# Kernel optimization log

Measured on AMD Instinct MI355X. Metric: run time of the kernel, lower is better.

## Reference

```python
import jax, jax.numpy as jnp
import numpy as np

D_MODEL = 1024
N_HEADS = 16
D_FF = 512  # FeedForward default d_ff=512 (not overridden in EncoderLayer)
EPS = 1e-6


def _norm(x, alpha, bias):
    # Custom NormLayer: mean + UNBIASED variance (torch.var default, N-1 denom)
    mean = jnp.mean(x, axis=-1, keepdims=True)
    n = x.shape[-1]
    var = jnp.sum((x - mean) ** 2, axis=-1, keepdims=True) / (n - 1)
    return alpha * (x - mean) / jnp.sqrt(var + EPS) + bias


def setup_inputs() -> dict:
    key = jax.random.key(0)
    ks = jax.random.split(key, 12)
    s = 1.0 / np.sqrt(D_MODEL)
    inp = {
        "x": jax.random.normal(ks[0], (2, 2048, D_MODEL), dtype=jnp.float32),
        "Wq": jax.random.uniform(ks[1], (D_MODEL, D_MODEL), jnp.float32, -s, s),
        "bq": jnp.zeros((D_MODEL,), jnp.float32),
        "Wk": jax.random.uniform(ks[2], (D_MODEL, D_MODEL), jnp.float32, -s, s),
        "bk": jnp.zeros((D_MODEL,), jnp.float32),
        "Wv": jax.random.uniform(ks[3], (D_MODEL, D_MODEL), jnp.float32, -s, s),
        "bv": jnp.zeros((D_MODEL,), jnp.float32),
        "Wo": jax.random.uniform(ks[4], (D_MODEL, D_MODEL), jnp.float32, -s, s),
        "bo": jnp.zeros((D_MODEL,), jnp.float32),
        "alpha1": jnp.ones((D_MODEL,), jnp.float32),
        "beta1": jnp.zeros((D_MODEL,), jnp.float32),
        "alpha2": jnp.ones((D_MODEL,), jnp.float32),
        "beta2": jnp.zeros((D_MODEL,), jnp.float32),
        "W1": jax.random.uniform(ks[5], (D_MODEL, D_FF), jnp.float32, -s, s),
        "b1": jnp.zeros((D_FF,), jnp.float32),
        "W2": jax.random.uniform(ks[6], (D_FF, D_MODEL), jnp.float32, -1.0 / np.sqrt(D_FF), 1.0 / np.sqrt(D_FF)),
        "b2": jnp.zeros((D_MODEL,), jnp.float32),
    }
    return inp


def reference(x, Wq, bq, Wk, bk, Wv, bv, Wo, bo, alpha1, beta1, alpha2, beta2, W1, b1, W2, b2):
    B, S, D = x.shape
    H = N_HEADS
    dh = D // H
    # norm_1 applied to x, result feeds BOTH attention and the residual
    x = _norm(x, alpha1, beta1)
    # multihead attention (dropout = identity in eval)
    q = (x @ Wq + bq).reshape(B, S, H, dh)
    k = (x @ Wk + bk).reshape(B, S, H, dh)
    v = (x @ Wv + bv).reshape(B, S, H, dh)
    scores = jnp.einsum("bqhd,bkhd->bhqk", q, k) / jnp.sqrt(jnp.asarray(dh, x.dtype))
    attn = jax.nn.softmax(scores, axis=-1)
    o = jnp.einsum("bhqk,bkhd->bqhd", attn, v).reshape(B, S, D)
    o = o @ Wo + bo
    x = x + o
    # FFN on norm_2(x)
    h = _norm(x, alpha2, beta2)
    h = jax.nn.relu(h @ W1 + b1) @ W2 + b2
    return x + h
```

## Files before the change

kernel.cpp:

```cpp
#include <hip/hip_runtime.h>

typedef __bf16 bf16;
typedef __bf16 bf16x4 __attribute__((ext_vector_type(4)));
typedef __bf16 bf16x8 __attribute__((ext_vector_type(8)));
typedef float f32x4 __attribute__((ext_vector_type(4)));

#define D_MODEL 1024
#define SEQ 2048
#define NB 2
#define LOG2E 1.4426950408889634f

__device__ __forceinline__ void glds16(const bf16* g, bf16* l) {
    __builtin_amdgcn_global_load_lds(
        (const __attribute__((address_space(1))) void*)g,
        (__attribute__((address_space(3))) void*)l, 16, 0, 0);
}

__device__ __forceinline__ void tile_tcvt(
    const float* __restrict__ src, int rows, int cols, bf16* __restrict__ dst,
    int bx, int by, bf16 (*t)[72])
{
    int tid = threadIdx.x;
    int k0 = by * 64, n0 = bx * 64;
    int r = tid >> 2, c = (tid & 3) * 16;
    const float4* s = (const float4*)(src + (size_t)(k0 + r) * cols + n0 + c);
#pragma unroll
    for (int q = 0; q < 4; ++q) {
        float4 v = s[q];
        t[c + q * 4 + 0][r] = (bf16)v.x;
        t[c + q * 4 + 1][r] = (bf16)v.y;
        t[c + q * 4 + 2][r] = (bf16)v.z;
        t[c + q * 4 + 3][r] = (bf16)v.w;
    }
    __syncthreads();
    bf16* d = dst + (size_t)(n0 + r) * rows + k0 + c;
    *(bf16x8*)(d)     = *(const bf16x8*)&t[r][c];
    *(bf16x8*)(d + 8) = *(const bf16x8*)&t[r][c + 8];
}

__global__ __launch_bounds__(256) void prep_kernel(
    const float* __restrict__ Wq, const float* __restrict__ Wk,
    const float* __restrict__ Wv, const float* __restrict__ Wo,
    const float* __restrict__ W1, const float* __restrict__ W2,
    const float* __restrict__ bq, const float* __restrict__ bk,
    const float* __restrict__ bv,
    bf16* __restrict__ Wqkv_t, bf16* __restrict__ Wo_t,
    bf16* __restrict__ W1_t, bf16* __restrict__ W2_t,
    float* __restrict__ b_qkv)
{
    __shared__ bf16 t[64][72];
    int id = blockIdx.x;
    if (id < 1024) {
        int which = id >> 8, tile = id & 255;
        const float* src = which == 0 ? Wq : which == 1 ? Wk : which == 2 ? Wv : Wo;
        bf16* dst = which == 3 ? Wo_t : Wqkv_t + (size_t)which * 1024 * 1024;
        tile_tcvt(src, 1024, 1024, dst, tile & 15, tile >> 4, t);
    } else if (id < 1152) {
        int tile = id - 1024;
        tile_tcvt(W1, 1024, 512, W1_t, tile & 7, tile >> 3, t);
    } else if (id < 1280) {
        int tile = id - 1152;
        tile_tcvt(W2, 512, 1024, W2_t, tile & 15, tile >> 4, t);
    } else {
        int i = (id - 1280) * 256 + threadIdx.x;
        float v;
        if (i < 1024) v = bq[i];
        else if (i < 2048) v = bk[i - 1024];
        else v = bv[i - 2048];
        b_qkv[i] = v;
    }
}

__global__ __launch_bounds__(256) void norm_kernel(
    const float* __restrict__ X, const float* __restrict__ alpha,
    const float* __restrict__ beta, bf16* __restrict__ Y)
{
    int row = blockIdx.x;
    int tid = threadIdx.x;
    float4 v = ((const float4*)(X + (size_t)row * D_MODEL))[tid];
    float s = v.x + v.y + v.z + v.w;
    float ss = v.x*v.x + v.y*v.y + v.z*v.z + v.w*v.w;
#pragma unroll
    for (int off = 1; off < 64; off <<= 1) {
        s  += __shfl_xor(s, off, 64);
        ss += __shfl_xor(ss, off, 64);
    }
    __shared__ float sd[8];
    int wave = tid >> 6, lane = tid & 63;
    if (lane == 0) { sd[wave] = s; sd[4 + wave] = ss; }
    __syncthreads();
    s  = sd[0] + sd[1] + sd[2] + sd[3];
    ss = sd[4] + sd[5] + sd[6] + sd[7];
    float mean = s * (1.0f / 1024.0f);
    float var  = (ss - s * mean) * (1.0f / 1023.0f);
    float rs = rsqrtf(var + 1e-6f);
    float4 a = ((const float4*)alpha)[tid];
    float4 bt = ((const float4*)beta)[tid];
    bf16x4 o;
    o[0] = (bf16)(a.x * (v.x - mean) * rs + bt.x);
    o[1] = (bf16)(a.y * (v.y - mean) * rs + bt.y);
    o[2] = (bf16)(a.z * (v.z - mean) * rs + bt.z);
    o[3] = (bf16)(a.w * (v.w - mean) * rs + bt.w);
    *(bf16x4*)(Y + (size_t)row * D_MODEL + tid * 4) = o;
}

__global__ __launch_bounds__(256) void crelu_kernel(
    const float* __restrict__ p0, const float* __restrict__ p1,
    const float* __restrict__ b1, bf16* __restrict__ h1)
{
    int i = blockIdx.x * 256 + threadIdx.x;
    float4 a = ((const float4*)p0)[i];
    float4 b = ((const float4*)p1)[i];
    int col = (i * 4) & 511;
    float4 bb = *(const float4*)(b1 + col);
    bf16x4 o;
    o[0] = (bf16)fmaxf(a.x + b.x + bb.x, 0.0f);
    o[1] = (bf16)fmaxf(a.y + b.y + bb.y, 0.0f);
    o[2] = (bf16)fmaxf(a.z + b.z + bb.z, 0.0f);
    o[3] = (bf16)fmaxf(a.w + b.w + bb.w, 0.0f);
    ((bf16x4*)h1)[i] = o;
}

template <typename OutT, int BN, int KU, bool VFUSE, bool SPLITK>
__global__ __launch_bounds__(256) void gemm128(
    const bf16* __restrict__ A, const bf16* __restrict__ Bt,
    const float* __restrict__ bias, const bf16* __restrict__ Rb,
    const float* __restrict__ Rf, OutT* __restrict__ C, bf16* __restrict__ vT,
    int M, int N, int K, int lda, int relu)
{
    constexpr int NT = BN / 32;
    constexpr int ASTR = 128 * 32;
    constexpr int BSTR = BN * 32;
    __shared__ bf16 As[ASTR * KU];
    __shared__ bf16 Bs[BSTR * KU];

    int tid = threadIdx.x;
    int wave = tid >> 6, lane = tid & 63;
    int quad = lane >> 4, l16 = lane & 15;
    int m0 = blockIdx.y * 128, n0 = blockIdx.x * BN;
    int wm = (wave >> 1) * 64, wn = (wave & 1) * (BN / 2);
    int Keff = SPLITK ? (K >> 1) : K;
    int klo  = SPLITK ? blockIdx.z * Keff : 0;

    f32x4 acc[4][NT] = {};

    const bf16* ga = A  + (size_t)(m0 + (tid >> 2)) * lda + (tid & 3) * 8 + klo;
    const bf16* gb = Bt + (size_t)(n0 + (tid >> 2)) * K   + (tid & 3) * 8 + klo;
    bf16* lAs = As + wave * 512;
    bf16* lBs = Bs + wave * 512;

    for (int k0 = 0; k0 < Keff; k0 += 32 * KU) {
        __syncthreads();
#pragma unroll
        for (int u = 0; u < KU; ++u) {
            glds16(ga + k0 + u * 32, lAs + u * ASTR);
            glds16(ga + (size_t)64 * lda + k0 + u * 32, lAs + u * ASTR + 2048);
            glds16(gb + k0 + u * 32, lBs + u * BSTR);
            if (BN == 128) glds16(gb + (size_t)64 * K + k0 + u * 32, lBs + u * BSTR + 2048);
        }
        __syncthreads();
#pragma unroll
        for (int u = 0; u < KU; ++u) {
            bf16x8 af[4], bfr[NT];
#pragma unroll
            for (int mt = 0; mt < 4; ++mt)
                af[mt] = *(const bf16x8*)(As + u * ASTR + (wm + mt * 16 + l16) * 32 + quad * 8);
#pragma unroll
            for (int nt = 0; nt < NT; ++nt)
                bfr[nt] = *(const bf16x8*)(Bs + u * BSTR + (wn + nt * 16 + l16) * 32 + quad * 8);
#pragma unroll
            for (int mt = 0; mt < 4; ++mt)
#pragma unroll
                for (int nt = 0; nt < NT; ++nt)
                    acc[mt][nt] = __builtin_amdgcn_mfma_f32_16x16x32_bf16(af[mt], bfr[nt], acc[mt][nt], 0, 0, 0);
        }
    }

    if (SPLITK) {
        float* P = (float*)C + (size_t)blockIdx.z * M * N;
#pragma unroll
        for (int nt = 0; nt < NT; ++nt) {
            int n = n0 + wn + nt * 16 + l16;
#pragma unroll
            for (int mt = 0; mt < 4; ++mt)
#pragma unroll
                for (int r = 0; r < 4; ++r) {
                    int m = m0 + wm + mt * 16 + quad * 4 + r;
                    P[(size_t)m * N + n] = acc[mt][nt][r];
                }
        }
        return;
    }

#pragma unroll
    for (int nt = 0; nt < NT; ++nt) {
        int n = n0 + wn + nt * 16 + l16;
        float bv = bias[n];
        if (VFUSE && n >= 2048) {
            int d = n & 63, h = (n - 2048) >> 6;
#pragma unroll
            for (int mt = 0; mt < 4; ++mt) {
                int m = m0 + wm + mt * 16 + quad * 4;
                int b = m >> 11, sidx = m & 2047;
                bf16x4 pk;
#pragma unroll
                for (int r = 0; r < 4; ++r) pk[r] = (bf16)(acc[mt][nt][r] + bv);
                *(bf16x4*)(vT + (((size_t)(b * 16 + h) * 64 + d) * SEQ + sidx)) = pk;
            }
        } else {
#pragma unroll
            for (int mt = 0; mt < 4; ++mt) {
#pragma unroll
                for (int r = 0; r < 4; ++r) {
                    int m = m0 + wm + mt * 16 + quad * 4 + r;
                    float vv = acc[mt][nt][r] + bv;
                    if (Rb) vv += (float)Rb[(size_t)m * N + n];
                    if (Rf) vv += Rf[(size_t)m * N + n];
                    if (relu) vv = vv > 0.0f ? vv : 0.0f;
                    C[(size_t)m * N + n] = (OutT)vv;
                }
            }
        }
    }
}

__global__ __launch_bounds__(512) void attn_kernel(
    const bf16* __restrict__ qkv, const bf16* __restrict__ vT, bf16* __restrict__ O)
{
    __shared__ bf16 Ks[64][72];
    __shared__ bf16 Vt[64][72];
    __shared__ bf16 Ps[8][16][72];

    int tid = threadIdx.x;
    int wave = tid >> 6, lane = tid & 63;
    int quad = lane >> 4, l16 = lane & 15;
    int bh = blockIdx.y, b = bh >> 4, h = bh & 15;
    int q0 = blockIdx.x * 128;

    const bf16* Qb = qkv + (size_t)(b * SEQ + q0 + wave * 16) * 3072 + h * 64;
    const bf16* Kb = qkv + (size_t)(b * SEQ) * 3072 + 1024 + h * 64;
    const bf16* Vb = vT + (size_t)bh * 64 * SEQ;

    const float c_l2 = 0.125f * LOG2E;
    bf16x8 qa[2];
#pragma unroll
    for (int hf = 0; hf < 2; ++hf) {
        bf16x8 raw = *(const bf16x8*)(Qb + (size_t)l16 * 3072 + hf * 32 + quad * 8);
        bf16x8 sc;
#pragma unroll
        for (int j = 0; j < 8; ++j) sc[j] = (bf16)((float)raw[j] * c_l2);
        qa[hf] = sc;
    }

    float lsum = 0.0f;
    f32x4 oacc[4] = {};

    int sr = tid >> 3, scol = (tid & 7) * 8;
    const bf16* kp = Kb + (size_t)sr * 3072 + scol;
    const bf16* vp = Vb + (size_t)sr * SEQ + scol;

    bf16x8 kr = *(const bf16x8*)kp;
    bf16x8 vr = *(const bf16x8*)vp;

    for (int kt = 0; kt < SEQ; kt += 64) {
        __syncthreads();
        *(bf16x8*)&Ks[sr][scol] = kr;
        *(bf16x8*)&Vt[sr][scol] = vr;
        __syncthreads();

        if (kt + 64 < SEQ) {
            kr = *(const bf16x8*)(kp + (size_t)(kt + 64) * 3072);
            vr = *(const bf16x8*)(vp + kt + 64);
        }

        bf16x8 kb[4][2], vb[4][2];
#pragma unroll
        for (int t4 = 0; t4 < 4; ++t4) {
            kb[t4][0] = *(const bf16x8*)&Ks[t4 * 16 + l16][quad * 8];
            kb[t4][1] = *(const bf16x8*)&Ks[t4 * 16 + l16][32 + quad * 8];
        }
#pragma unroll
        for (int dt = 0; dt < 4; ++dt) {
            vb[dt][0] = *(const bf16x8*)&Vt[dt * 16 + l16][quad * 8];
            vb[dt][1] = *(const bf16x8*)&Vt[dt * 16 + l16][32 + quad * 8];
        }
#pragma unroll
        for (int t4 = 0; t4 < 4; ++t4) {
            f32x4 c = {};
            c = __builtin_amdgcn_mfma_f32_16x16x32_bf16(kb[t4][0], qa[0], c, 0, 0, 0);
            c = __builtin_amdgcn_mfma_f32_16x16x32_bf16(kb[t4][1], qa[1], c, 0, 0, 0);
            bf16x4 pk;
            float psum = 0.0f;
#pragma unroll
            for (int r = 0; r < 4; ++r) {
                float p = exp2f(c[r]);
                psum += p;
                pk[r] = (bf16)p;
            }
            lsum += psum;
            *(bf16x4*)&Ps[wave][l16][t4 * 16 + quad * 4] = pk;
        }
        bf16x8 pa0 = *(const bf16x8*)&Ps[wave][l16][quad * 8];
        bf16x8 pa1 = *(const bf16x8*)&Ps[wave][l16][32 + quad * 8];
#pragma unroll
        for (int dt = 0; dt < 4; ++dt) {
            oacc[dt] = __builtin_amdgcn_mfma_f32_16x16x32_bf16(pa0, vb[dt][0], oacc[dt], 0, 0, 0);
            oacc[dt] = __builtin_amdgcn_mfma_f32_16x16x32_bf16(pa1, vb[dt][1], oacc[dt], 0, 0, 0);
        }
    }
    float lr = lsum;
    lr += __shfl_xor(lr, 16);
    lr += __shfl_xor(lr, 32);
#pragma unroll
    for (int r = 0; r < 4; ++r) {
        float inv = 1.0f / __shfl(lr, quad * 4 + r, 16);
        int row = b * SEQ + q0 + wave * 16 + quad * 4 + r;
        bf16* op = O + (size_t)row * D_MODEL + h * 64;
#pragma unroll
        for (int dt = 0; dt < 4; ++dt)
            op[dt * 16 + l16] = (bf16)(oacc[dt][r] * inv);
    }
}

extern "C" void kernel_launch(void* const* d_in, const int* in_sizes, int n_in,
                              void* d_out, int out_size, void* d_ws, size_t ws_size,
                              hipStream_t stream)
{
    const float* x      = (const float*)d_in[0];
    const float* Wq     = (const float*)d_in[1];
    const float* bq     = (const float*)d_in[2];
    const float* Wk     = (const float*)d_in[3];
    const float* bk     = (const float*)d_in[4];
    const float* Wv     = (const float*)d_in[5];
    const float* bv     = (const float*)d_in[6];
    const float* Wo     = (const float*)d_in[7];
    const float* bo     = (const float*)d_in[8];
    const float* alpha1 = (const float*)d_in[9];
    const float* beta1  = (const float*)d_in[10];
    const float* alpha2 = (const float*)d_in[11];
    const float* beta2  = (const float*)d_in[12];
    const float* W1     = (const float*)d_in[13];
    const float* b1     = (const float*)d_in[14];
    const float* W2     = (const float*)d_in[15];
    const float* b2     = (const float*)d_in[16];

    char* ws = (char*)d_ws;
    const size_t MB = 1ull << 20;
    bf16*  Wqkv_t = (bf16*)(ws + 0 * MB);
    bf16*  Wo_t   = (bf16*)(ws + 6 * MB);
    bf16*  W1_t   = (bf16*)(ws + 8 * MB);
    bf16*  W2_t   = (bf16*)(ws + 9 * MB);
    float* b_qkv  = (float*)(ws + 10 * MB);
    bf16*  xn     = (bf16*)(ws + 11 * MB);
    bf16*  qkv    = (bf16*)(ws + 19 * MB);
    bf16*  vT     = (bf16*)(ws + 43 * MB);
    bf16*  o      = (bf16*)(ws + 51 * MB);
    float* x2     = (float*)(ws + 19 * MB);
    bf16*  hn     = (bf16*)(ws + 35 * MB);
    float* pF1    = (float*)(ws + 43 * MB);
    bf16*  h1     = (bf16*)(ws + 11 * MB);

    const int M = NB * SEQ;

    prep_kernel<<<1292, 256, 0, stream>>>(Wq, Wk, Wv, Wo, W1, W2, bq, bk, bv,
                                          Wqkv_t, Wo_t, W1_t, W2_t, b_qkv);

    norm_kernel<<<M, 256, 0, stream>>>(x, alpha1, beta1, xn);

    gemm128<bf16, 128, 2, true, false><<<dim3(24, 32), 256, 0, stream>>>(
        xn, Wqkv_t, b_qkv, nullptr, nullptr, qkv, vT, M, 3072, D_MODEL, D_MODEL, 0);

    attn_kernel<<<dim3(SEQ / 128, 32), 512, 0, stream>>>(qkv, vT, o);

    gemm128<float, 64, 1, false, false><<<dim3(16, 32), 256, 0, stream>>>(
        o, Wo_t, bo, xn, nullptr, x2, nullptr, M, D_MODEL, D_MODEL, D_MODEL, 0);

    norm_kernel<<<M, 256, 0, stream>>>(x2, alpha2, beta2, hn);

    gemm128<float, 64, 1, false, true><<<dim3(8, 32, 2), 256, 0, stream>>>(
        hn, W1_t, nullptr, nullptr, nullptr, pF1, nullptr, M, 512, D_MODEL, D_MODEL, 0);

    crelu_kernel<<<(M * 512) / 1024, 256, 0, stream>>>(
        pF1, pF1 + (size_t)M * 512, b1, h1);

    gemm128<float, 64, 1, false, false><<<dim3(16, 32), 256, 0, stream>>>(
        h1, W2_t, b2, nullptr, x2, (float*)d_out, nullptr, M, D_MODEL, 512, 512, 0);
}
```

Baseline: 282.3 us.

## Split attention key tiles across wave pairs and retune GEMM template parameter

The attention kernel now gives each wave 32 query rows and half of each 64-key tile, not 16 rows and the whole tile. The two partial outputs and row sums are combined through shared memory at the end. This raises K-fragment reuse across two query subtiles and halves the V fragments each wave loads, at the cost of a final shared-memory reduction and extra syncs. Separately, the Wo, W1 and W2 GEMM launches switch a template parameter from 1 to 2, likely a pipelining stage or occupancy setting.

```diff
diff --git a/kernel.cpp b/kernel.cpp
--- a/kernel.cpp
+++ b/kernel.cpp
@@ -227,98 +227,137 @@
 __global__ __launch_bounds__(512) void attn_kernel(
     const bf16* __restrict__ qkv, const bf16* __restrict__ vT, bf16* __restrict__ O)
 {
-    __shared__ bf16 Ks[64][72];
-    __shared__ bf16 Vt[64][72];
-    __shared__ bf16 Ps[8][16][72];
+    __shared__ __align__(16) char smem[38912];
+    bf16* Ks = (bf16*)smem;
+    bf16* Vt = (bf16*)(smem + 9216);
+    bf16* Ps = (bf16*)(smem + 18432);
 
     int tid = threadIdx.x;
     int wave = tid >> 6, lane = tid & 63;
     int quad = lane >> 4, l16 = lane & 15;
+    int qg = wave >> 1, kg = wave & 1;
     int bh = blockIdx.y, b = bh >> 4, h = bh & 15;
-    int q0 = blockIdx.x * 128;
-
-    const bf16* Qb = qkv + (size_t)(b * SEQ + q0 + wave * 16) * 3072 + h * 64;
+    int q0 = blockIdx.x * 128 + qg * 32;
+
+    const bf16* Qb = qkv + (size_t)(b * SEQ + q0) * 3072 + h * 64;
     const bf16* Kb = qkv + (size_t)(b * SEQ) * 3072 + 1024 + h * 64;
     const bf16* Vb = vT + (size_t)bh * 64 * SEQ;
 
     const float c_l2 = 0.125f * LOG2E;
-    bf16x8 qa[2];
-#pragma unroll
-    for (int hf = 0; hf < 2; ++hf) {
-        bf16x8 raw = *(const bf16x8*)(Qb + (size_t)l16 * 3072 + hf * 32 + quad * 8);
-        bf16x8 sc;
-#pragma unroll
-        for (int j = 0; j < 8; ++j) sc[j] = (bf16)((float)raw[j] * c_l2);
-        qa[hf] = sc;
-    }
-
-    float lsum = 0.0f;
-    f32x4 oacc[4] = {};
+    bf16x8 qa[2][2];
+#pragma unroll
+    for (int mt = 0; mt < 2; ++mt)
+#pragma unroll
+        for (int hf = 0; hf < 2; ++hf) {
+            bf16x8 raw = *(const bf16x8*)(Qb + (size_t)(mt * 16 + l16) * 3072 + hf * 32 + quad * 8);
+            bf16x8 sc;
+#pragma unroll
+            for (int j = 0; j < 8; ++j) sc[j] = (bf16)((float)raw[j] * c_l2);
+            qa[mt][hf] = sc;
+        }
+
+    float lsum[2] = {};
+    f32x4 oacc[2][4] = {};
 
     int sr = tid >> 3, scol = (tid & 7) * 8;
     const bf16* kp = Kb + (size_t)sr * 3072 + scol;
     const bf16* vp = Vb + (size_t)sr * SEQ + scol;
-
     bf16x8 kr = *(const bf16x8*)kp;
     bf16x8 vr = *(const bf16x8*)vp;
 
+    bf16* PsW = Ps + wave * 32 * 40;
+    const bf16* KsKg = Ks + kg * 32 * 72;
+
     for (int kt = 0; kt < SEQ; kt += 64) {
         __syncthreads();
-        *(bf16x8*)&Ks[sr][scol] = kr;
-        *(bf16x8*)&Vt[sr][scol] = vr;
+        *(bf16x8*)(Ks + sr * 72 + scol) = kr;
+        *(bf16x8*)(Vt + sr * 72 + scol) = vr;
         __syncthreads();
-
         if (kt + 64 < SEQ) {
             kr = *(const bf16x8*)(kp + (size_t)(kt + 64) * 3072);
             vr = *(const bf16x8*)(vp + kt + 64);
         }
 
-        bf16x8 kb[4][2], vb[4][2];
-#pragma unroll
-        for (int t4 = 0; t4 < 4; ++t4) {
-            kb[t4][0] = *(const bf16x8*)&Ks[t4 * 16 + l16][quad * 8];
-            kb[t4][1] = *(const bf16x8*)&Ks[t4 * 16 + l16][32 + quad * 8];
-        }
-#pragma unroll
-        for (int dt = 0; dt < 4; ++dt) {
-            vb[dt][0] = *(const bf16x8*)&Vt[dt * 16 + l16][quad * 8];
-            vb[dt][1] = *(const bf16x8*)&Vt[dt * 16 + l16][32 + quad * 8];
-        }
-#pragma unroll
-        for (int t4 = 0; t4 < 4; ++t4) {
-            f32x4 c = {};
-            c = __builtin_amdgcn_mfma_f32_16x16x32_bf16(kb[t4][0], qa[0], c, 0, 0, 0);
-            c = __builtin_amdgcn_mfma_f32_16x16x32_bf16(kb[t4][1], qa[1], c, 0, 0, 0);
-            bf16x4 pk;
-            float psum = 0.0f;
+        bf16x8 kb[2][2], vb[4];
+#pragma unroll
+        for (int t4 = 0; t4 < 2; ++t4) {
+            kb[t4][0] = *(const bf16x8*)(KsKg + (t4 * 16 + l16) * 72 + quad * 8);
+            kb[t4][1] = *(const bf16x8*)(KsKg + (t4 * 16 + l16) * 72 + 32 + quad * 8);
+        }
+#pragma unroll
+        for (int dt = 0; dt < 4; ++dt)
+            vb[dt] = *(const bf16x8*)(Vt + (dt * 16 + l16) * 72 + kg * 32 + quad * 8);
+
+#pragma unroll
+        for (int mt = 0; mt < 2; ++mt)
+#pragma unroll
+            for (int t4 = 0; t4 < 2; ++t4) {
+                f32x4 c = {};
+                c = __builtin_amdgcn_mfma_f32_16x16x32_bf16(kb[t4][0], qa[mt][0], c, 0, 0, 0);
+                c = __builtin_amdgcn_mfma_f32_16x16x32_bf16(kb[t4][1], qa[mt][1], c, 0, 0, 0);
+                bf16x4 pk;
+                float psum = 0.0f;
+#pragma unroll
+                for (int r = 0; r < 4; ++r) {
+                    float p = exp2f(c[r]);
+                    psum += p;
+                    pk[r] = (bf16)p;
+                }
+                lsum[mt] += psum;
+                *(bf16x4*)(PsW + (mt * 16 + l16) * 40 + t4 * 16 + quad * 4) = pk;
+            }
+#pragma unroll
+        for (int mt = 0; mt < 2; ++mt) {
+            bf16x8 pa = *(const bf16x8*)(PsW + (mt * 16 + l16) * 40 + quad * 8);
+#pragma unroll
+            for (int dt = 0; dt < 4; ++dt)
+                oacc[mt][dt] = __builtin_amdgcn_mfma_f32_16x16x32_bf16(pa, vb[dt], oacc[mt][dt], 0, 0, 0);
+        }
+    }
+
+    float lr[2];
+#pragma unroll
+    for (int mt = 0; mt < 2; ++mt) {
+        lr[mt] = lsum[mt];
+        lr[mt] += __shfl_xor(lr[mt], 16);
+        lr[mt] += __shfl_xor(lr[mt], 32);
+    }
+    __syncthreads();
+    float* sf = (float*)smem;
+    float* lb = sf + 8192;
+    if (kg == 1) {
+#pragma unroll
+        for (int mt = 0; mt < 2; ++mt)
+#pragma unroll
+            for (int dt = 0; dt < 4; ++dt)
+                *(f32x4*)&sf[qg * 2048 + (dt * 16 + l16) * 32 + mt * 16 + quad * 4] = oacc[mt][dt];
+        if (lane < 16) {
+            lb[(qg * 2 + 0) * 16 + l16] = lr[0];
+            lb[(qg * 2 + 1) * 16 + l16] = lr[1];
+        }
+    }
+    __syncthreads();
+    if (kg == 0) {
+#pragma unroll
+        for (int mt = 0; mt < 2; ++mt) {
+            lr[mt] += lb[(qg * 2 + mt) * 16 + l16];
+#pragma unroll
+            for (int dt = 0; dt < 4; ++dt) {
+                f32x4 other = *(const f32x4*)&sf[qg * 2048 + (dt * 16 + l16) * 32 + mt * 16 + quad * 4];
+                oacc[mt][dt] += other;
+            }
+        }
+#pragma unroll
+        for (int mt = 0; mt < 2; ++mt)
 #pragma unroll
             for (int r = 0; r < 4; ++r) {
-                float p = exp2f(c[r]);
-                psum += p;
-                pk[r] = (bf16)p;
+                float inv = 1.0f / __shfl(lr[mt], quad * 4 + r, 16);
+                int row = b * SEQ + q0 + mt * 16 + quad * 4 + r;
+                bf16* op = O + (size_t)row * D_MODEL + h * 64;
+#pragma unroll
+                for (int dt = 0; dt < 4; ++dt)
+                    op[dt * 16 + l16] = (bf16)(oacc[mt][dt][r] * inv);
             }
-            lsum += psum;
-            *(bf16x4*)&Ps[wave][l16][t4 * 16 + quad * 4] = pk;
-        }
-        bf16x8 pa0 = *(const bf16x8*)&Ps[wave][l16][quad * 8];
-        bf16x8 pa1 = *(const bf16x8*)&Ps[wave][l16][32 + quad * 8];
-#pragma unroll
-        for (int dt = 0; dt < 4; ++dt) {
-            oacc[dt] = __builtin_amdgcn_mfma_f32_16x16x32_bf16(pa0, vb[dt][0], oacc[dt], 0, 0, 0);
-            oacc[dt] = __builtin_amdgcn_mfma_f32_16x16x32_bf16(pa1, vb[dt][1], oacc[dt], 0, 0, 0);
-        }
-    }
-    float lr = lsum;
-    lr += __shfl_xor(lr, 16);
-    lr += __shfl_xor(lr, 32);
-#pragma unroll
-    for (int r = 0; r < 4; ++r) {
-        float inv = 1.0f / __shfl(lr, quad * 4 + r, 16);
-        int row = b * SEQ + q0 + wave * 16 + quad * 4 + r;
-        bf16* op = O + (size_t)row * D_MODEL + h * 64;
-#pragma unroll
-        for (int dt = 0; dt < 4; ++dt)
-            op[dt * 16 + l16] = (bf16)(oacc[dt][r] * inv);
     }
 }
 
@@ -372,17 +411,17 @@
 
     attn_kernel<<<dim3(SEQ / 128, 32), 512, 0, stream>>>(qkv, vT, o);
 
-    gemm128<float, 64, 1, false, false><<<dim3(16, 32), 256, 0, stream>>>(
+    gemm128<float, 64, 2, false, false><<<dim3(16, 32), 256, 0, stream>>>(
         o, Wo_t, bo, xn, nullptr, x2, nullptr, M, D_MODEL, D_MODEL, D_MODEL, 0);
 
     norm_kernel<<<M, 256, 0, stream>>>(x2, alpha2, beta2, hn);
 
-    gemm128<float, 64, 1, false, true><<<dim3(8, 32, 2), 256, 0, stream>>>(
+    gemm128<float, 64, 2, false, true><<<dim3(8, 32, 2), 256, 0, stream>>>(
         hn, W1_t, nullptr, nullptr, nullptr, pF1, nullptr, M, 512, D_MODEL, D_MODEL, 0);
 
     crelu_kernel<<<(M * 512) / 1024, 256, 0, stream>>>(
         pF1, pF1 + (size_t)M * 512, b1, h1);
 
-    gemm128<float, 64, 1, false, false><<<dim3(16, 32), 256, 0, stream>>>(
+    gemm128<float, 64, 2, false, false><<<dim3(16, 32), 256, 0, stream>>>(
         h1, W2_t, b2, nullptr, x2, (float*)d_out, nullptr, M, D_MODEL, 512, 512, 0);
 }
```

After: 269.1 us. -4.7%, faster.
